# Optimization experiments

Measured on AMD Instinct MI355X. Metric: run time of the kernel, lower is better.

## Reference

```python
import jax, jax.numpy as jnp
import numpy as np

NUM_USERS, NUM_ITEMS, RANK = 610, 193609, 4
BATCH = 2097152


def setup_inputs() -> dict:
    key = jax.random.key(0)
    ks = jax.random.split(key, 10)
    users = jax.random.randint(ks[0], (BATCH,), 0, NUM_USERS + 1)
    items = jax.random.randint(ks[1], (BATCH,), 0, NUM_ITEMS + 1)
    # embedding tables (nn.Embedding default init ~ N(0,1))
    embed_U = jax.random.normal(ks[2], (NUM_USERS + 1, RANK), dtype=jnp.float32)
    embed_V = jax.random.normal(ks[3], (NUM_ITEMS + 1, RANK), dtype=jnp.float32)
    # Linear params, Kaiming-uniform-ish scale (1/sqrt(fan_in))
    def lin(k, fan_in, fan_out):
        k1, k2 = jax.random.split(k)
        bound = 1.0 / np.sqrt(fan_in)
        W = jax.random.uniform(k1, (fan_out, fan_in), jnp.float32, -bound, bound)
        b = jax.random.uniform(k2, (fan_out,), jnp.float32, -bound, bound)
        return W, b
    W1, b1 = lin(ks[4], 2 * RANK, 50)
    W2, b2 = lin(ks[5], 50, 20)
    W3, b3 = lin(ks[6], 20, 1)
    return {"users": users, "items": items,
            "embed_U": embed_U, "embed_V": embed_V,
            "W1": W1, "b1": b1, "W2": W2, "b2": b2, "W3": W3, "b3": b3}


def reference(users, items, embed_U, embed_V, W1, b1, W2, b2, W3, b3):
    # Vectorized version of the per-sample loop: gather + concat + 3-layer MLP
    eu = embed_U[users]                      # [B, rank]
    ev = embed_V[items]                      # [B, rank]
    x = jnp.concatenate([eu, ev], axis=-1)   # [B, 2*rank]
    x = jax.nn.relu(x @ W1.T + b1)           # [B, 50]
    x = jax.nn.relu(x @ W2.T + b2)           # [B, 20]
    x = x @ W3.T + b3                        # [B, 1]
    return x[:, 0]                           # [B]
```

## Files before the change

### kernel.cpp

```cpp
#include <hip/hip_runtime.h>
#include <hip/hip_fp16.h>


typedef __attribute__((ext_vector_type(16))) float    f32x16;
typedef __attribute__((ext_vector_type(8)))  _Float16 f16x8;
typedef __attribute__((ext_vector_type(2)))  __fp16   h16x2;

#define H1 50
#define H2 20

union W4 { unsigned u[4]; f16x8 v; };
union W8 { _Float16 h[8]; f16x8 v; };

static __device__ inline unsigned pk_u32(float a, float b) {
    h16x2 p = __builtin_amdgcn_cvt_pkrtz(a, b);
    unsigned u; __builtin_memcpy(&u, &p, 4); return u;
}
static __device__ inline unsigned pkmax0(unsigned a) {
    unsigned r;
    asm("v_pk_max_f16 %0, %1, %2" : "=v"(r) : "v"(a), "v"(0u));
    return r;
}

__global__ __launch_bounds__(256, 4) void neumf_mfma32(
    const int* __restrict__ users, const int* __restrict__ items,
    const float* __restrict__ eU, const float* __restrict__ eV,
    const float* __restrict__ W1, const float* __restrict__ b1,
    const float* __restrict__ W2, const float* __restrict__ b2,
    const float* __restrict__ W3, const float* __restrict__ b3,
    float* __restrict__ out, int n, int nTiles, int tilesPerWave, int nU)
{
    const int lane = threadIdx.x & 63;
    const int wid  = blockIdx.x * (blockDim.x >> 6) + (threadIdx.x >> 6);
    const int h    = lane >> 5;
    const int r31  = lane & 31;

    __shared__ uint2 ldsU[616];
    for (int r = threadIdx.x; r < nU; r += 256) {
        float4 t = reinterpret_cast<const float4*>(eU)[r];
        ldsU[r] = make_uint2(pk_u32(t.x, t.y), pk_u32(t.z, t.w));
    }
    __syncthreads();

    f16x8 a1[2];
#pragma unroll
    for (int mt = 0; mt < 2; ++mt) {
        int m = 32 * mt + r31;
        float w[8] = {0.f,0.f,0.f,0.f,0.f,0.f,0.f,0.f};
        if (m < H1) {
#pragma unroll
            for (int i = 0; i < 4; ++i) w[i] = W1[m * 8 + 4 * h + i];
            if (h == 0) w[4] = b1[m];
        }
        W8 f;
#pragma unroll
        for (int i = 0; i < 8; ++i) f.h[i] = (_Float16)w[i];
        a1[mt] = f.v;
    }

    f16x8 a2[4];
    {
        int m = r31;
#pragma unroll
        for (int kt = 0; kt < 4; ++kt) {
            float w[8] = {0.f,0.f,0.f,0.f,0.f,0.f,0.f,0.f};
            if (m < H2) {
#pragma unroll
                for (int e = 0; e < 8; ++e) {
                    int k = 16 * kt + 4 * h + (e & 3) + 8 * (e >> 2);
                    if (k < H1)       w[e] = W2[m * H1 + k];
                    else if (k == H1) w[e] = b2[m];
                }
            }
            W8 f;
#pragma unroll
            for (int e = 0; e < 8; ++e) f.h[e] = (_Float16)w[e];
            a2[kt] = f.v;
        }
    }

    f16x8 a3;
    {
        W8 f;
#pragma unroll
        for (int e = 0; e < 8; ++e) {
            int k = 4 * h + (e & 3) + 8 * (e >> 2);
            f.h[e] = (_Float16)W3[k];
        }
        a3 = f.v;
    }
    float w3t[4];
#pragma unroll
    for (int j = 0; j < 4; ++j) w3t[j] = h ? 0.f : W3[16 + j];
    const float bias3 = b3[0];

    const int*     ip  = h ? items : users;
    const unsigned w2c = h ? 0u : 0x00003C00u;

    const int t0 = wid * tilesPerWave;
    const int t1 = min(t0 + tilesPerWave, nTiles);
    if (t0 >= t1) return;

    int idx_cur = ip[32 * t0 + r31];
    float4 gv_cur;
    if (h) gv_cur = *reinterpret_cast<const float4*>(eV + 4 * (size_t)idx_cur);
    int idx_next = ip[32 * min(t0 + 1, t1 - 1) + r31];

    for (int T = t0; T < t1; ++T) {
        float4 gv_next;
        if (h) gv_next = *reinterpret_cast<const float4*>(eV + 4 * (size_t)idx_next);
        int idx_nn = ip[32 * min(T + 2, t1 - 1) + r31];

        uint2 cw;
        if (h) cw = make_uint2(pk_u32(gv_cur.x, gv_cur.y), pk_u32(gv_cur.z, gv_cur.w));
        else   cw = ldsU[idx_cur];

        W4 bf1;
        bf1.u[0] = cw.x;
        bf1.u[1] = cw.y;
        bf1.u[2] = w2c;
        bf1.u[3] = 0u;

        f32x16 z = {0.f,0.f,0.f,0.f,0.f,0.f,0.f,0.f,0.f,0.f,0.f,0.f,0.f,0.f,0.f,0.f};
        f32x16 d1[2];
        d1[0] = __builtin_amdgcn_mfma_f32_32x32x16_f16(a1[0], bf1.v, z, 0, 0, 0);
        d1[1] = __builtin_amdgcn_mfma_f32_32x32x16_f16(a1[1], bf1.v, z, 0, 0, 0);

        d1[1][10] = h ? d1[1][10] : 1.0f;

        f32x16 d2 = z;
#pragma unroll
        for (int kt = 0; kt < 4; ++kt) {
            const int mt = kt >> 1, q = kt & 1;
            W4 bf;
#pragma unroll
            for (int j = 0; j < 4; ++j)
                bf.u[j] = pkmax0(pk_u32(d1[mt][8 * q + 2 * j], d1[mt][8 * q + 2 * j + 1]));
            d2 = __builtin_amdgcn_mfma_f32_32x32x16_f16(a2[kt], bf.v, d2, 0, 0, 0);
        }

        W4 b3f;
        b3f.u[0] = pkmax0(pk_u32(d2[0], d2[1]));
        b3f.u[1] = pkmax0(pk_u32(d2[2], d2[3]));
        b3f.u[2] = pkmax0(pk_u32(d2[4], d2[5]));
        b3f.u[3] = pkmax0(pk_u32(d2[6], d2[7]));
        f32x16 d3 = __builtin_amdgcn_mfma_f32_32x32x16_f16(a3, b3f.v, z, 0, 0, 0);

        float pt = bias3;
#pragma unroll
        for (int j = 0; j < 4; ++j)
            pt = fmaf(fmaxf(d2[8 + j], 0.f), w3t[j], pt);

        if (!h) out[32 * T + r31] = d3[0] + pt;

        gv_cur = gv_next; idx_cur = idx_next; idx_next = idx_nn;
    }
}

extern "C" void kernel_launch(void* const* d_in, const int* in_sizes, int n_in,
                              void* d_out, int out_size, void* d_ws, size_t ws_size,
                              hipStream_t stream) {
    const int*   users = (const int*)d_in[0];
    const int*   items = (const int*)d_in[1];
    const float* eU    = (const float*)d_in[2];
    const float* eV    = (const float*)d_in[3];
    const float* W1    = (const float*)d_in[4];
    const float* b1    = (const float*)d_in[5];
    const float* W2    = (const float*)d_in[6];
    const float* b2    = (const float*)d_in[7];
    const float* W3    = (const float*)d_in[8];
    const float* b3    = (const float*)d_in[9];
    float*       out   = (float*)d_out;

    int n  = in_sizes[0];
    int nU = in_sizes[2] / 4;

    int nTiles = (n + 31) / 32;
    int blocks = 1024, threads = 256;
    int totalWaves = blocks * (threads / 64);
    int tilesPerWave = (nTiles + totalWaves - 1) / totalWaves;
    neumf_mfma32<<<blocks, threads, 0, stream>>>(users, items, eU, eV,
                                                 W1, b1, W2, b2, W3, b3,
                                                 out, n, nTiles, tilesPerWave, nU);
}
```

Measured before the change: 23.68 us.

## Switch MLP from 32x32x16 MFMA to 16x16x32 tiles with dot2 final layer

Restructures the per-tile MLP to process 16 samples per wave using 16x16x32 f16 MFMAs instead of 32 samples with 32x32x16 MFMAs. The weight fragments are re-laid out, and the third layer is computed with packed fdot2 plus cross-lane shuffles instead of an MFMA. Occupancy hint and block count are raised. The aim is to cut wasted MFMA work on padded dimensions and shorten the dependency chain, at the cost of more loop iterations and shuffle overhead.

Result: slower. 39.36 us (+66.2%).

```diff
diff --git a/kernel.cpp b/kernel.cpp
--- a/kernel.cpp
+++ b/kernel.cpp
@@ -2,9 +2,10 @@
 #include <hip/hip_fp16.h>
 
 
-typedef __attribute__((ext_vector_type(16))) float    f32x16;
-typedef __attribute__((ext_vector_type(8)))  _Float16 f16x8;
-typedef __attribute__((ext_vector_type(2)))  __fp16   h16x2;
+typedef __attribute__((ext_vector_type(4))) float    f32x4;
+typedef __attribute__((ext_vector_type(8))) _Float16 f16x8;
+typedef __attribute__((ext_vector_type(2))) _Float16 f16x2;
+typedef __attribute__((ext_vector_type(2))) __fp16   h16x2;
 
 #define H1 50
 #define H2 20
@@ -21,8 +22,14 @@
     asm("v_pk_max_f16 %0, %1, %2" : "=v"(r) : "v"(a), "v"(0u));
     return r;
 }
+static __device__ inline float dot2(unsigned a, unsigned b, float c) {
+    f16x2 av, bv;
+    __builtin_memcpy(&av, &a, 4);
+    __builtin_memcpy(&bv, &b, 4);
+    return __builtin_amdgcn_fdot2(av, bv, c, false);
+}
 
-__global__ __launch_bounds__(256, 4) void neumf_mfma32(
+__global__ __launch_bounds__(256, 5) void neumf_mfma16(
     const int* __restrict__ users, const int* __restrict__ items,
     const float* __restrict__ eU, const float* __restrict__ eV,
     const float* __restrict__ W1, const float* __restrict__ b1,
@@ -32,8 +39,8 @@
 {
     const int lane = threadIdx.x & 63;
     const int wid  = blockIdx.x * (blockDim.x >> 6) + (threadIdx.x >> 6);
-    const int h    = lane >> 5;
-    const int r31  = lane & 31;
+    const int g    = lane >> 4;
+    const int r15  = lane & 15;
 
     __shared__ uint2 ldsU[616];
     for (int r = threadIdx.x; r < nU; r += 256) {
@@ -42,116 +49,115 @@
     }
     __syncthreads();
 
-    f16x8 a1[2];
+    f16x8 a1[4];
 #pragma unroll
-    for (int mt = 0; mt < 2; ++mt) {
-        int m = 32 * mt + r31;
-        float w[8] = {0.f,0.f,0.f,0.f,0.f,0.f,0.f,0.f};
-        if (m < H1) {
-#pragma unroll
-            for (int i = 0; i < 4; ++i) w[i] = W1[m * 8 + 4 * h + i];
-            if (h == 0) w[4] = b1[m];
-        }
+    for (int mt = 0; mt < 4; ++mt) {
+        int m = 16 * mt + r15;
         W8 f;
 #pragma unroll
-        for (int i = 0; i < 8; ++i) f.h[i] = (_Float16)w[i];
+        for (int e = 0; e < 8; ++e) {
+            int k = 4 * g + (e & 3) + 16 * (e >> 2);
+            float w = 0.f;
+            if (m < H1) {
+                if (k < 8)       w = W1[m * 8 + k];
+                else if (k == 8) w = b1[m];
+            }
+            f.h[e] = (_Float16)w;
+        }
         a1[mt] = f.v;
     }
 
-    f16x8 a2[4];
-    {
-        int m = r31;
+    f16x8 a2[2][2];
 #pragma unroll
-        for (int kt = 0; kt < 4; ++kt) {
-            float w[8] = {0.f,0.f,0.f,0.f,0.f,0.f,0.f,0.f};
-            if (m < H2) {
+    for (int mt = 0; mt < 2; ++mt) {
 #pragma unroll
-                for (int e = 0; e < 8; ++e) {
-                    int k = 16 * kt + 4 * h + (e & 3) + 8 * (e >> 2);
-                    if (k < H1)       w[e] = W2[m * H1 + k];
-                    else if (k == H1) w[e] = b2[m];
-                }
-            }
+        for (int kt = 0; kt < 2; ++kt) {
+            int m = 16 * mt + r15;
             W8 f;
 #pragma unroll
-            for (int e = 0; e < 8; ++e) f.h[e] = (_Float16)w[e];
-            a2[kt] = f.v;
+            for (int e = 0; e < 8; ++e) {
+                int k = 32 * kt + 4 * g + (e & 3) + 16 * (e >> 2);
+                float w = 0.f;
+                if (m < H2) {
+                    if (k < H1)       w = W2[m * H1 + k];
+                    else if (k == H1) w = b2[m];
+                }
+                f.h[e] = (_Float16)w;
+            }
+            a2[mt][kt] = f.v;
         }
     }
 
-    f16x8 a3;
-    {
-        W8 f;
-#pragma unroll
-        for (int e = 0; e < 8; ++e) {
-            int k = 4 * h + (e & 3) + 8 * (e >> 2);
-            f.h[e] = (_Float16)W3[k];
-        }
-        a3 = f.v;
-    }
-    float w3t[4];
-#pragma unroll
-    for (int j = 0; j < 4; ++j) w3t[j] = h ? 0.f : W3[16 + j];
+    const unsigned w3a = pk_u32(W3[4 * g], W3[4 * g + 1]);
+    const unsigned w3b = pk_u32(W3[4 * g + 2], W3[4 * g + 3]);
+    const unsigned w3c = (g == 0) ? pk_u32(W3[16], W3[17]) : 0u;
+    const unsigned w3d = (g == 0) ? pk_u32(W3[18], W3[19]) : 0u;
     const float bias3 = b3[0];
 
-    const int*     ip  = h ? items : users;
-    const unsigned w2c = h ? 0u : 0x00003C00u;
+    const int* ip = (g == 1) ? items : users;
+    const unsigned gconst = (g == 2) ? 0x00003C00u : 0u;
 
     const int t0 = wid * tilesPerWave;
     const int t1 = min(t0 + tilesPerWave, nTiles);
     if (t0 >= t1) return;
+    const int tl = t1 - 1;
 
-    int idx_cur = ip[32 * t0 + r31];
+    int idx_cur = 0, idx_next = 0;
+    if (g < 2) idx_cur = ip[16 * t0 + r15];
     float4 gv_cur;
-    if (h) gv_cur = *reinterpret_cast<const float4*>(eV + 4 * (size_t)idx_cur);
-    int idx_next = ip[32 * min(t0 + 1, t1 - 1) + r31];
+    if (g == 1) gv_cur = *reinterpret_cast<const float4*>(eV + 4 * (size_t)idx_cur);
+    if (g < 2) idx_next = ip[16 * min(t0 + 1, tl) + r15];
 
     for (int T = t0; T < t1; ++T) {
         float4 gv_next;
-        if (h) gv_next = *reinterpret_cast<const float4*>(eV + 4 * (size_t)idx_next);
-        int idx_nn = ip[32 * min(T + 2, t1 - 1) + r31];
+        if (g == 1) gv_next = *reinterpret_cast<const float4*>(eV + 4 * (size_t)idx_next);
+        int idx_nn = 0;
+        if (g < 2) idx_nn = ip[16 * min(T + 2, tl) + r15];
 
         uint2 cw;
-        if (h) cw = make_uint2(pk_u32(gv_cur.x, gv_cur.y), pk_u32(gv_cur.z, gv_cur.w));
-        else   cw = ldsU[idx_cur];
+        if (g == 0) cw = ldsU[idx_cur];
+        else if (g == 1) cw = make_uint2(pk_u32(gv_cur.x, gv_cur.y),
+                                         pk_u32(gv_cur.z, gv_cur.w));
+        else cw = make_uint2(gconst, 0u);
 
         W4 bf1;
         bf1.u[0] = cw.x;
         bf1.u[1] = cw.y;
-        bf1.u[2] = w2c;
+        bf1.u[2] = 0u;
         bf1.u[3] = 0u;
 
-        f32x16 z = {0.f,0.f,0.f,0.f,0.f,0.f,0.f,0.f,0.f,0.f,0.f,0.f,0.f,0.f,0.f,0.f};
-        f32x16 d1[2];
-        d1[0] = __builtin_amdgcn_mfma_f32_32x32x16_f16(a1[0], bf1.v, z, 0, 0, 0);
-        d1[1] = __builtin_amdgcn_mfma_f32_32x32x16_f16(a1[1], bf1.v, z, 0, 0, 0);
+        f32x4 z4 = {0.f, 0.f, 0.f, 0.f};
+        f32x4 d1[4];
+#pragma unroll
+        for (int mt = 0; mt < 4; ++mt)
+            d1[mt] = __builtin_amdgcn_mfma_f32_16x16x32_f16(a1[mt], bf1.v, z4, 0, 0, 0);
 
-        d1[1][10] = h ? d1[1][10] : 1.0f;
+        W4 bk0, bk1;
+        bk0.u[0] = pkmax0(pk_u32(d1[0][0], d1[0][1]));
+        bk0.u[1] = pkmax0(pk_u32(d1[0][2], d1[0][3]));
+        bk0.u[2] = pkmax0(pk_u32(d1[1][0], d1[1][1]));
+        bk0.u[3] = pkmax0(pk_u32(d1[1][2], d1[1][3]));
+        bk1.u[0] = pkmax0(pk_u32(d1[2][0], d1[2][1]));
+        bk1.u[1] = pkmax0(pk_u32(d1[2][2], d1[2][3]));
+        bk1.u[2] = pkmax0(pk_u32(d1[3][0], d1[3][1]));
+        bk1.u[3] = (g == 0) ? 0x00003C00u
+                            : pkmax0(pk_u32(d1[3][2], d1[3][3]));
 
-        f32x16 d2 = z;
-#pragma unroll
-        for (int kt = 0; kt < 4; ++kt) {
-            const int mt = kt >> 1, q = kt & 1;
-            W4 bf;
-#pragma unroll
-            for (int j = 0; j < 4; ++j)
-                bf.u[j] = pkmax0(pk_u32(d1[mt][8 * q + 2 * j], d1[mt][8 * q + 2 * j + 1]));
-            d2 = __builtin_amdgcn_mfma_f32_32x32x16_f16(a2[kt], bf.v, d2, 0, 0, 0);
-        }
+        f32x4 d2a, d2b;
+        d2a = __builtin_amdgcn_mfma_f32_16x16x32_f16(a2[0][0], bk0.v, z4, 0, 0, 0);
+        d2a = __builtin_amdgcn_mfma_f32_16x16x32_f16(a2[0][1], bk1.v, d2a, 0, 0, 0);
+        d2b = __builtin_amdgcn_mfma_f32_16x16x32_f16(a2[1][0], bk0.v, z4, 0, 0, 0);
+        d2b = __builtin_amdgcn_mfma_f32_16x16x32_f16(a2[1][1], bk1.v, d2b, 0, 0, 0);
 
-        W4 b3f;
-        b3f.u[0] = pkmax0(pk_u32(d2[0], d2[1]));
-        b3f.u[1] = pkmax0(pk_u32(d2[2], d2[3]));
-        b3f.u[2] = pkmax0(pk_u32(d2[4], d2[5]));
-        b3f.u[3] = pkmax0(pk_u32(d2[6], d2[7]));
-        f32x16 d3 = __builtin_amdgcn_mfma_f32_32x32x16_f16(a3, b3f.v, z, 0, 0, 0);
+        unsigned pa = pkmax0(pk_u32(d2a[0], d2a[1]));
+        unsigned pb = pkmax0(pk_u32(d2a[2], d2a[3]));
+        unsigned pc = pkmax0(pk_u32(d2b[0], d2b[1]));
+        unsigned pd = pkmax0(pk_u32(d2b[2], d2b[3]));
+        float pt = dot2(pa, w3a, dot2(pb, w3b, dot2(pc, w3c, dot2(pd, w3d, 0.f))));
+        pt += __shfl_xor(pt, 16, 64);
+        pt += __shfl_xor(pt, 32, 64);
 
-        float pt = bias3;
-#pragma unroll
-        for (int j = 0; j < 4; ++j)
-            pt = fmaf(fmaxf(d2[8 + j], 0.f), w3t[j], pt);
-
-        if (!h) out[32 * T + r31] = d3[0] + pt;
+        if (g == 0) out[16 * T + r15] = pt + bias3;
 
         gv_cur = gv_next; idx_cur = idx_next; idx_next = idx_nn;
     }
@@ -175,11 +181,11 @@
     int n  = in_sizes[0];
     int nU = in_sizes[2] / 4;
 
-    int nTiles = (n + 31) / 32;
-    int blocks = 1024, threads = 256;
+    int nTiles = (n + 15) / 16;
+    int blocks = 1280, threads = 256;
     int totalWaves = blocks * (threads / 64);
     int tilesPerWave = (nTiles + totalWaves - 1) / totalWaves;
-    neumf_mfma32<<<blocks, threads, 0, stream>>>(users, items, eU, eV,
+    neumf_mfma16<<<blocks, threads, 0, stream>>>(users, items, eU, eV,
                                                  W1, b1, W2, b2, W3, b3,
                                                  out, n, nTiles, tilesPerWave, nU);
 }
```
